# Performance work log

Hardware: AMD Instinct MI355X
Metric: run time of the kernel (lower is better)

The kernel has to match this reference:

```python
import jax, jax.numpy as jnp
import numpy as np

N_HEADS = 16
N_KV_HEADS = 4
HEAD_DIM = 128


def apply_rope(x, cos, sin):
    # x: [b, h, s, head_dim]; cos/sin: [1, 1, s, head_dim//2]
    d = x.shape[-1] // 2
    x1, x2 = x[..., :d], x[..., d:]
    return jnp.concatenate([x1 * cos - x2 * sin, x1 * sin + x2 * cos], axis=-1)


def setup_inputs() -> dict:
    key = jax.random.key(0)
    ks = jax.random.split(key, 9)
    b, s, dim = 2, 2048, 2048
    inp = {
        "x": jax.random.normal(ks[0], (b, s, dim), jnp.float32),
        "cos": jax.random.normal(ks[1], (1, 1, s, HEAD_DIM // 2), jnp.float32),
        "sin": jax.random.normal(ks[2], (1, 1, s, HEAD_DIM // 2), jnp.float32),
        "Wq": jax.random.normal(ks[3], (dim, N_HEADS * HEAD_DIM), jnp.float32) * 0.02,
        "bq": jax.random.normal(ks[4], (N_HEADS * HEAD_DIM,), jnp.float32) * 0.02,
        "Wkv": jax.random.normal(ks[5], (dim, 2 * N_KV_HEADS * HEAD_DIM), jnp.float32) * 0.02,
        "bkv": jax.random.normal(ks[6], (2 * N_KV_HEADS * HEAD_DIM,), jnp.float32) * 0.02,
        "Wo": jax.random.normal(ks[7], (N_HEADS * HEAD_DIM, dim), jnp.float32) * 0.02,
        "bo": jax.random.normal(ks[8], (dim,), jnp.float32) * 0.02,
        "causal": 1,
    }
    return inp


def reference(x, cos, sin, Wq, bq, Wkv, bkv, Wo, bo, causal):
    b, s, dim = x.shape
    scale = 1.0 / np.sqrt(HEAD_DIM)
    # QKV projections (torch Linear with weight stored transposed here)
    q = (x @ Wq + bq).reshape(b, s, N_HEADS, HEAD_DIM).transpose(0, 2, 1, 3)
    kv = x @ Wkv + bkv  # [b, s, 2*n_kv*hd]
    k, v = jnp.split(kv, 2, axis=-1)
    k = k.reshape(b, s, N_KV_HEADS, HEAD_DIM).transpose(0, 2, 1, 3)
    v = v.reshape(b, s, N_KV_HEADS, HEAD_DIM).transpose(0, 2, 1, 3)
    q = apply_rope(q, cos, sin)
    k = apply_rope(k, cos, sin)
    # GQA: repeat kv heads
    rep = N_HEADS // N_KV_HEADS
    k = jnp.repeat(k, rep, axis=1)
    v = jnp.repeat(v, rep, axis=1)
    logits = jnp.einsum("bhqd,bhkd->bhqk", q, k) * scale
    if causal:
        mask = jnp.tril(jnp.ones((s, s), dtype=bool))
        logits = jnp.where(mask[None, None], logits, jnp.finfo(logits.dtype).min)
    scores = jax.nn.softmax(logits, axis=-1)
    vo = jnp.einsum("bhqk,bhkd->bhqd", scores, v)
    vo = vo.transpose(0, 2, 1, 3).reshape(b, s, N_HEADS * HEAD_DIM)
    out = vo @ Wo + bo
    return out
```

## Files before the change

kernel.cpp:

```cpp
#include <hip/hip_runtime.h>
#include <hip/hip_bf16.h>

typedef __bf16 bf16x8 __attribute__((ext_vector_type(8)));
typedef float  f32x4  __attribute__((ext_vector_type(4)));
typedef unsigned int u32;

#define GLD_LDS16(gp, lp) __builtin_amdgcn_global_load_lds( \
    (const __attribute__((address_space(1))) u32*)(gp), \
    (__attribute__((address_space(3))) u32*)(lp), 16, 0, 0)

template<int CTRL>
__device__ __forceinline__ float dpp_rot(float x) {
    int y = __builtin_amdgcn_update_dpp(__float_as_int(x), __float_as_int(x),
                                        CTRL, 0xF, 0xF, false);
    return __int_as_float(y);
}
__device__ __forceinline__ float rowmax16(float x) {
    x = fmaxf(x, dpp_rot<0x121>(x));
    x = fmaxf(x, dpp_rot<0x122>(x));
    x = fmaxf(x, dpp_rot<0x124>(x));
    x = fmaxf(x, dpp_rot<0x128>(x));
    return x;
}
__device__ __forceinline__ float rowsum16(float x) {
    x += dpp_rot<0x121>(x);
    x += dpp_rot<0x122>(x);
    x += dpp_rot<0x124>(x);
    x += dpp_rot<0x128>(x);
    return x;
}


__global__ __launch_bounds__(256) void f32_to_bf16_kernel(
    const float* __restrict__ in, __bf16* __restrict__ out, size_t n) {
    size_t i = ((size_t)blockIdx.x * 256 + threadIdx.x) * 8;
    if (i >= n) return;
    float4 a = *(const float4*)(in + i);
    float4 b = *(const float4*)(in + i + 4);
    bf16x8 v;
    v[0] = (__bf16)a.x; v[1] = (__bf16)a.y; v[2] = (__bf16)a.z; v[3] = (__bf16)a.w;
    v[4] = (__bf16)b.x; v[5] = (__bf16)b.y; v[6] = (__bf16)b.z; v[7] = (__bf16)b.w;
    *(bf16x8*)(out + i) = v;
}

__global__ __launch_bounds__(256) void transpose_to_bf16_kernel(
    const float* __restrict__ W, __bf16* __restrict__ Wt, int K, int N) {
    __shared__ float tile[32][33];
    int n0 = blockIdx.x * 32, k0 = blockIdx.y * 32;
    int tx = threadIdx.x, ty = threadIdx.y;
    #pragma unroll
    for (int i = 0; i < 32; i += 8)
        tile[ty + i][tx] = W[(size_t)(k0 + ty + i) * N + n0 + tx];
    __syncthreads();
    #pragma unroll
    for (int i = 0; i < 32; i += 8)
        Wt[(size_t)(n0 + ty + i) * K + k0 + tx] = (__bf16)tile[tx][ty + i];
}

__global__ __launch_bounds__(256) void concat_bias_kernel(
    const float* __restrict__ bq, const float* __restrict__ bkv,
    float* __restrict__ bqkv) {
    int i = blockIdx.x * 256 + threadIdx.x;
    if (i < 2048) bqkv[i] = bq[i];
    else if (i < 3072) bqkv[i] = bkv[i - 2048];
}

__global__ __launch_bounds__(256) void transpose_v_kernel(
    const __bf16* __restrict__ qkv, __bf16* __restrict__ vtg, int S) {
    __shared__ __bf16 tile[32][33];
    int s0 = blockIdx.x * 32, d0 = blockIdx.y * 32, z = blockIdx.z;
    int b = z >> 2, kvh = z & 3;
    int tx = threadIdx.x, ty = threadIdx.y;
    #pragma unroll
    for (int i = 0; i < 32; i += 8)
        tile[ty + i][tx] =
            qkv[((size_t)b * S + s0 + ty + i) * 3072 + 2560 + kvh * 128 + d0 + tx];
    __syncthreads();
    #pragma unroll
    for (int i = 0; i < 32; i += 8)
        vtg[((size_t)z * 128 + d0 + ty + i) * S + s0 + tx] = tile[tx][ty + i];
}

#define BM 128
#define BN 128
#define BK 64

template <typename OutT>
__global__ __launch_bounds__(256) void gemm_bt_bias_kernel(
    const __bf16* __restrict__ A, const __bf16* __restrict__ Bt,
    const float* __restrict__ bias, OutT* __restrict__ C,
    int M, int N, int K) {
    __shared__ __bf16 As[BM * BK];
    __shared__ __bf16 Bs[BN * BK];
    int tid  = threadIdx.x;
    int nwg  = gridDim.x;
    int cpx  = nwg >> 3;
    int swzb = (blockIdx.x & 7) * cpx + (blockIdx.x >> 3);
    int nbm  = M / BM;
    int bm   = swzb % nbm;
    int bn   = swzb / nbm;
    int wave = tid >> 6;
    int lane = tid & 63;
    int wm   = (wave >> 1) * 64;
    int wn   = (wave & 1) * 64;
    int quad = lane >> 4;
    int l16  = lane & 15;
    int gr   = wave * 32 + (lane >> 3);
    int gc   = (lane & 7) * 8;

    f32x4 acc[4][4];
    f32x4 zero = {0.f, 0.f, 0.f, 0.f};
    #pragma unroll
    for (int i = 0; i < 4; ++i)
        #pragma unroll
        for (int j = 0; j < 4; ++j) acc[i][j] = zero;

    const __bf16* Abase = A  + (size_t)(bm * BM) * K;
    const __bf16* Bbase = Bt + (size_t)(bn * BN) * K;

    for (int k0 = 0; k0 < K; k0 += BK) {
        if (k0) __syncthreads();
        #pragma unroll
        for (int i = 0; i < 4; ++i) {
            GLD_LDS16(Abase + (size_t)(gr + i * 8) * K + k0 + gc,
                      &As[(wave * 32 + i * 8) * BK]);
            GLD_LDS16(Bbase + (size_t)(gr + i * 8) * K + k0 + gc,
                      &Bs[(wave * 32 + i * 8) * BK]);
        }
        __syncthreads();

        bf16x8 af[4][2], bf[4][2];
        #pragma unroll
        for (int i = 0; i < 4; ++i)
            #pragma unroll
            for (int kc = 0; kc < 2; ++kc)
                af[i][kc] = *(bf16x8*)&As[(wm + i * 16 + l16) * BK + kc * 32 + quad * 8];
        #pragma unroll
        for (int j = 0; j < 4; ++j)
            #pragma unroll
            for (int kc = 0; kc < 2; ++kc)
                bf[j][kc] = *(bf16x8*)&Bs[(wn + j * 16 + l16) * BK + kc * 32 + quad * 8];
        #pragma unroll
        for (int kc = 0; kc < 2; ++kc)
            #pragma unroll
            for (int i = 0; i < 4; ++i)
                #pragma unroll
                for (int j = 0; j < 4; ++j)
                    acc[i][j] = __builtin_amdgcn_mfma_f32_16x16x32_bf16(
                        af[i][kc], bf[j][kc], acc[i][j], 0, 0, 0);
    }

    #pragma unroll
    for (int i = 0; i < 4; ++i) {
        int row = bm * BM + wm + i * 16 + quad * 4;
        #pragma unroll
        for (int j = 0; j < 4; ++j) {
            int col  = bn * BN + wn + j * 16 + l16;
            float bv = bias[col];
            #pragma unroll
            for (int r = 0; r < 4; ++r)
                C[(size_t)(row + r) * N + col] = (OutT)(acc[i][j][r] + bv);
        }
    }
}

__global__ __launch_bounds__(256) void rope_kernel(
    __bf16* __restrict__ buf, const float* __restrict__ cosp,
    const float* __restrict__ sinp, int heads, int rowstride, int coloff,
    int S, int total) {
    int idx = blockIdx.x * 256 + threadIdx.x;
    if (idx >= total) return;
    int d  = idx & 63;
    int t2 = idx >> 6;
    int h  = t2 % heads;
    int r  = t2 / heads;
    int s  = r & (S - 1);
    size_t base = (size_t)r * rowstride + coloff + h * 128;
    float x1 = (float)buf[base + d];
    float x2 = (float)buf[base + d + 64];
    float c  = cosp[s * 64 + d];
    float sn = sinp[s * 64 + d];
    buf[base + d]      = (__bf16)(x1 * c - x2 * sn);
    buf[base + d + 64] = (__bf16)(x1 * sn + x2 * c);
}


__global__ __launch_bounds__(256) void flash_mfma_kernel(
    const __bf16* __restrict__ qkv,
    const __bf16* __restrict__ vtg,
    __bf16* __restrict__ vo,
    const int* __restrict__ causal_p, int S) {
    __shared__ __bf16 Ks[2][64 * 128];
    __shared__ __bf16 Vs[2][64 * 128];
    __shared__ __bf16 Ps[4 * 16 * 64];

    const int QKV = 3072;
    int tid  = threadIdx.x;
    int wave = tid >> 6;
    int lane = tid & 63;
    int quad = lane >> 4;
    int l16  = lane & 15;
    int id   = blockIdx.x;
    int xcd  = id & 7;
    int b    = xcd >> 2;
    int kvh  = xcd & 3;
    int rest = id >> 3;
    int hh   = rest & 3;
    int pair = rest >> 2;
    int h    = kvh * 4 + hh;
    int causal = causal_p[0];
    const float SCALE = 0.08838834764831845f;

    const __bf16* vB = vtg + ((size_t)(b * 4 + kvh) * 128) * S;
    char* psw = (char*)Ps + wave * 2048;

    #pragma unroll 1
    for (int phase = 0; phase < 2; ++phase) {
        int qt = phase ? (31 - pair) : pair;
        int q0 = qt * 64;
        int nt = causal ? (qt + 1) : (S / 64);

        bf16x8 a_frag[4];
        size_t qrow = ((size_t)b * S + q0 + wave * 16 + l16) * QKV + h * 128 + quad * 8;
        #pragma unroll
        for (int kc = 0; kc < 4; ++kc)
            a_frag[kc] = *(const bf16x8*)(qkv + qrow + kc * 32);

        f32x4 o_acc[8];
        f32x4 zero4 = {0.f, 0.f, 0.f, 0.f};
        #pragma unroll
        for (int dt = 0; dt < 8; ++dt) o_acc[dt] = zero4;
        float m_[4], l_[4];
        #pragma unroll
        for (int r = 0; r < 4; ++r) { m_[r] = -1e30f; l_[r] = 0.f; }
        int qrow_d = q0 + wave * 16 + quad * 4;

        __syncthreads();
        {
            size_t kg = ((size_t)b * S + wave * 16 + l16) * QKV + 2048 + kvh * 128 + quad * 8;
            #pragma unroll
            for (int kc = 0; kc < 4; ++kc)
                GLD_LDS16(qkv + kg + kc * 32, &Ks[0][(wave * 4 + kc) * 512]);
            #pragma unroll
            for (int i = 0; i < 4; ++i) {
                int c  = wave * 4 + i;
                int dt = c >> 1, kc = c & 1;
                GLD_LDS16(vB + (size_t)(dt * 16 + l16) * S + kc * 32 + quad * 8,
                          &Vs[0][c * 512]);
            }
        }

        for (int t = 0; t < nt; ++t) {
            int cur = t & 1;
            __syncthreads();
            if (t + 1 < nt) {
                size_t kg = ((size_t)b * S + (t + 1) * 64 + wave * 16 + l16) * QKV
                            + 2048 + kvh * 128 + quad * 8;
                #pragma unroll
                for (int kc = 0; kc < 4; ++kc)
                    GLD_LDS16(qkv + kg + kc * 32, &Ks[1 - cur][(wave * 4 + kc) * 512]);
                size_t vgoff = (size_t)(t + 1) * 64;
                #pragma unroll
                for (int i = 0; i < 4; ++i) {
                    int c  = wave * 4 + i;
                    int dt = c >> 1, kc = c & 1;
                    GLD_LDS16(vB + (size_t)(dt * 16 + l16) * S + vgoff + kc * 32 + quad * 8,
                              &Vs[1 - cur][c * 512]);
                }
            }
            int j0 = t * 64;

            f32x4 s_t[4];
            #pragma unroll
            for (int jt = 0; jt < 4; ++jt) s_t[jt] = zero4;
            #pragma unroll
            for (int jt = 0; jt < 4; ++jt)
                #pragma unroll
                for (int kc = 0; kc < 4; ++kc) {
                    bf16x8 kf = *(bf16x8*)&Ks[cur][(jt * 4 + kc) * 512 + lane * 8];
                    s_t[jt] = __builtin_amdgcn_mfma_f32_16x16x32_bf16(
                        a_frag[kc], kf, s_t[jt], 0, 0, 0);
                }

            int diag = causal && (t == nt - 1);
            #pragma unroll
            for (int jt = 0; jt < 4; ++jt)
                #pragma unroll
                for (int r = 0; r < 4; ++r) {
                    float sv = s_t[jt][r] * SCALE;
                    if (diag && (j0 + jt * 16 + l16 > qrow_d + r)) sv = -1e30f;
                    s_t[jt][r] = sv;
                }

            float alpha[4];
            #pragma unroll
            for (int r = 0; r < 4; ++r) {
                float v = fmaxf(fmaxf(s_t[0][r], s_t[1][r]),
                                fmaxf(s_t[2][r], s_t[3][r]));
                v = rowmax16(v);
                float m_new = fmaxf(m_[r], v);
                alpha[r] = __expf(m_[r] - m_new);
                m_[r] = m_new;
                float rs = 0.f;
                #pragma unroll
                for (int jt = 0; jt < 4; ++jt) {
                    float p = __expf(s_t[jt][r] - m_new);
                    s_t[jt][r] = p;
                    rs += p;
                }
                l_[r] = l_[r] * alpha[r] + rs;
            }
            #pragma unroll
            for (int jt = 0; jt < 4; ++jt)
                #pragma unroll
                for (int r = 0; r < 4; ++r) {
                    int prow = quad * 4 + r;
                    int inb  = (jt * 16 + l16) * 2;
                    *(__bf16*)(psw + prow * 128 + (inb ^ ((prow & 7) << 4))) =
                        (__bf16)s_t[jt][r];
                }
            #pragma unroll
            for (int dt = 0; dt < 8; ++dt)
                #pragma unroll
                for (int r = 0; r < 4; ++r) o_acc[dt][r] *= alpha[r];

            int rb  = l16 * 128;
            int swz = (l16 & 7) << 4;
            bf16x8 p0 = *(bf16x8*)(psw + rb + ((quad * 16) ^ swz));
            bf16x8 p1 = *(bf16x8*)(psw + rb + ((64 + quad * 16) ^ swz));
            #pragma unroll
            for (int dt = 0; dt < 8; ++dt) {
                bf16x8 vf0 = *(bf16x8*)&Vs[cur][(dt * 2 + 0) * 512 + lane * 8];
                bf16x8 vf1 = *(bf16x8*)&Vs[cur][(dt * 2 + 1) * 512 + lane * 8];
                o_acc[dt] = __builtin_amdgcn_mfma_f32_16x16x32_bf16(
                    p0, vf0, o_acc[dt], 0, 0, 0);
                o_acc[dt] = __builtin_amdgcn_mfma_f32_16x16x32_bf16(
                    p1, vf1, o_acc[dt], 0, 0, 0);
            }
        }

        float invl[4];
        #pragma unroll
        for (int r = 0; r < 4; ++r) invl[r] = 1.f / rowsum16(l_[r]);
        size_t obase = ((size_t)b * S + q0 + wave * 16 + quad * 4) * 2048
                       + h * 128 + l16;
        #pragma unroll
        for (int dt = 0; dt < 8; ++dt)
            #pragma unroll
            for (int r = 0; r < 4; ++r)
                vo[obase + (size_t)r * 2048 + dt * 16] = (__bf16)(o_acc[dt][r] * invl[r]);
    }
}


extern "C" void kernel_launch(void* const* d_in, const int* in_sizes, int n_in,
                              void* d_out, int out_size, void* d_ws, size_t ws_size,
                              hipStream_t stream) {
    const float* x    = (const float*)d_in[0];
    const float* cosp = (const float*)d_in[1];
    const float* sinp = (const float*)d_in[2];
    const float* Wq   = (const float*)d_in[3];
    const float* bq   = (const float*)d_in[4];
    const float* Wkv  = (const float*)d_in[5];
    const float* bkv  = (const float*)d_in[6];
    const float* Wo   = (const float*)d_in[7];
    const float* bo   = (const float*)d_in[8];
    const int* causal = (const int*)d_in[9];
    float* out = (float*)d_out;

    const int B = 2, S = 2048;
    const int M = B * S;

    char* w = (char*)d_ws;
    __bf16* x16    = (__bf16*)w; w += (size_t)M * 2048 * 2;
    __bf16* Wqkvt  = (__bf16*)w; w += (size_t)3072 * 2048 * 2;
    __bf16* Wot    = (__bf16*)w; w += (size_t)2048 * 2048 * 2;
    float*  bqkv   = (float*)w;  w += (size_t)3072 * 4;
    __bf16* qkvbuf = (__bf16*)w; w += (size_t)M * 3072 * 2;
    __bf16* vobuf  = x16;
    __bf16* vtg    = Wqkvt;

    f32_to_bf16_kernel<<<(M * 2048) / (256 * 8), 256, 0, stream>>>(x, x16, (size_t)M * 2048);
    transpose_to_bf16_kernel<<<dim3(2048 / 32, 2048 / 32), dim3(32, 8), 0, stream>>>(Wq, Wqkvt, 2048, 2048);
    transpose_to_bf16_kernel<<<dim3(1024 / 32, 2048 / 32), dim3(32, 8), 0, stream>>>(Wkv, Wqkvt + (size_t)2048 * 2048, 2048, 1024);
    transpose_to_bf16_kernel<<<dim3(2048 / 32, 2048 / 32), dim3(32, 8), 0, stream>>>(Wo, Wot, 2048, 2048);
    concat_bias_kernel<<<12, 256, 0, stream>>>(bq, bkv, bqkv);
    gemm_bt_bias_kernel<__bf16><<<dim3((M / BM) * (3072 / BN)), 256, 0, stream>>>(x16, Wqkvt, bqkv, qkvbuf, M, 3072, 2048);
    {
        int totq = M * 16 * 64;
        rope_kernel<<<(totq + 255) / 256, 256, 0, stream>>>(qkvbuf, cosp, sinp, 16, 3072, 0, S, totq);
        int totk = M * 4 * 64;
        rope_kernel<<<(totk + 255) / 256, 256, 0, stream>>>(qkvbuf, cosp, sinp, 4, 3072, 2048, S, totk);
    }
    transpose_v_kernel<<<dim3(S / 32, 128 / 32, B * 4), dim3(32, 8), 0, stream>>>(qkvbuf, vtg, S);
    flash_mfma_kernel<<<dim3(512), 256, 0, stream>>>(qkvbuf, vtg, vobuf, causal, S);
    gemm_bt_bias_kernel<float><<<dim3((M / BM) * (2048 / BN)), 256, 0, stream>>>(vobuf, Wot, bo, out, M, 2048, 2048);
}
```

Measured before the change: 393.2 us.

## Fuse prep kernels, fold RoPE and V-transpose into QKV GEMM epilogue

Merges the x conversion, three weight transposes and bias concat into one multi-role prep kernel, cutting launches. The QKV GEMM now stages its output tile in LDS and applies RoPE to Q/K in the epilogue, writing V directly in transposed layout. This removes the separate rope and V-transpose passes and their extra global round-trips, and shrinks the QKV row stride to 2560. It also adds s_setprio around the MFMA blocks in the flash kernel, and gives vtg its own workspace region instead of aliasing the weights.

```diff
diff --git a/kernel.cpp b/kernel.cpp
--- a/kernel.cpp
+++ b/kernel.cpp
@@ -30,68 +30,93 @@
     return x;
 }
 
-
-__global__ __launch_bounds__(256) void f32_to_bf16_kernel(
-    const float* __restrict__ in, __bf16* __restrict__ out, size_t n) {
-    size_t i = ((size_t)blockIdx.x * 256 + threadIdx.x) * 8;
-    if (i >= n) return;
-    float4 a = *(const float4*)(in + i);
-    float4 b = *(const float4*)(in + i + 4);
-    bf16x8 v;
-    v[0] = (__bf16)a.x; v[1] = (__bf16)a.y; v[2] = (__bf16)a.z; v[3] = (__bf16)a.w;
-    v[4] = (__bf16)b.x; v[5] = (__bf16)b.y; v[6] = (__bf16)b.z; v[7] = (__bf16)b.w;
-    *(bf16x8*)(out + i) = v;
-}
-
-__global__ __launch_bounds__(256) void transpose_to_bf16_kernel(
-    const float* __restrict__ W, __bf16* __restrict__ Wt, int K, int N) {
-    __shared__ float tile[32][33];
-    int n0 = blockIdx.x * 32, k0 = blockIdx.y * 32;
-    int tx = threadIdx.x, ty = threadIdx.y;
-    #pragma unroll
-    for (int i = 0; i < 32; i += 8)
-        tile[ty + i][tx] = W[(size_t)(k0 + ty + i) * N + n0 + tx];
-    __syncthreads();
-    #pragma unroll
-    for (int i = 0; i < 32; i += 8)
-        Wt[(size_t)(n0 + ty + i) * K + k0 + tx] = (__bf16)tile[tx][ty + i];
-}
-
-__global__ __launch_bounds__(256) void concat_bias_kernel(
+#define NPREP_A 4096
+#define NPREP_B 4096
+#define NPREP_C 2048
+#define NPREP_D 4096
+#define NPREP_E 12
+
+__global__ __launch_bounds__(256) void prep_kernel(
+    const float* __restrict__ x, __bf16* __restrict__ x16,
+    const float* __restrict__ Wq, const float* __restrict__ Wkv,
+    const float* __restrict__ Wo,
+    __bf16* __restrict__ Wqkvt, __bf16* __restrict__ Wot,
     const float* __restrict__ bq, const float* __restrict__ bkv,
     float* __restrict__ bqkv) {
-    int i = blockIdx.x * 256 + threadIdx.x;
-    if (i < 2048) bqkv[i] = bq[i];
-    else if (i < 3072) bqkv[i] = bkv[i - 2048];
-}
-
-__global__ __launch_bounds__(256) void transpose_v_kernel(
-    const __bf16* __restrict__ qkv, __bf16* __restrict__ vtg, int S) {
-    __shared__ __bf16 tile[32][33];
-    int s0 = blockIdx.x * 32, d0 = blockIdx.y * 32, z = blockIdx.z;
-    int b = z >> 2, kvh = z & 3;
-    int tx = threadIdx.x, ty = threadIdx.y;
-    #pragma unroll
-    for (int i = 0; i < 32; i += 8)
-        tile[ty + i][tx] =
-            qkv[((size_t)b * S + s0 + ty + i) * 3072 + 2560 + kvh * 128 + d0 + tx];
-    __syncthreads();
-    #pragma unroll
-    for (int i = 0; i < 32; i += 8)
-        vtg[((size_t)z * 128 + d0 + ty + i) * S + s0 + tx] = tile[tx][ty + i];
+    __shared__ float tile[32][33];
+    int bid = blockIdx.x;
+    int tid = threadIdx.x;
+
+    if (bid < NPREP_A) {
+        size_t i = (size_t)bid * 2048 + tid * 8;
+        float4 a = *(const float4*)(x + i);
+        float4 b = *(const float4*)(x + i + 4);
+        bf16x8 v;
+        v[0] = (__bf16)a.x; v[1] = (__bf16)a.y; v[2] = (__bf16)a.z; v[3] = (__bf16)a.w;
+        v[4] = (__bf16)b.x; v[5] = (__bf16)b.y; v[6] = (__bf16)b.z; v[7] = (__bf16)b.w;
+        *(bf16x8*)(x16 + i) = v;
+        return;
+    }
+    bid -= NPREP_A;
+    int tx = tid & 31, ty = tid >> 5;
+
+    if (bid < NPREP_B) {
+        int n0 = (bid & 63) * 32, k0 = (bid >> 6) * 32;
+        #pragma unroll
+        for (int i = 0; i < 32; i += 8)
+            tile[ty + i][tx] = Wq[(size_t)(k0 + ty + i) * 2048 + n0 + tx];
+        __syncthreads();
+        #pragma unroll
+        for (int i = 0; i < 32; i += 8)
+            Wqkvt[(size_t)(n0 + ty + i) * 2048 + k0 + tx] = (__bf16)tile[tx][ty + i];
+        return;
+    }
+    bid -= NPREP_B;
+    if (bid < NPREP_C) {
+        int n0 = (bid & 31) * 32, k0 = (bid >> 5) * 32;
+        #pragma unroll
+        for (int i = 0; i < 32; i += 8)
+            tile[ty + i][tx] = Wkv[(size_t)(k0 + ty + i) * 1024 + n0 + tx];
+        __syncthreads();
+        #pragma unroll
+        for (int i = 0; i < 32; i += 8)
+            Wqkvt[(size_t)(2048 + n0 + ty + i) * 2048 + k0 + tx] = (__bf16)tile[tx][ty + i];
+        return;
+    }
+    bid -= NPREP_C;
+    if (bid < NPREP_D) {
+        int n0 = (bid & 63) * 32, k0 = (bid >> 6) * 32;
+        #pragma unroll
+        for (int i = 0; i < 32; i += 8)
+            tile[ty + i][tx] = Wo[(size_t)(k0 + ty + i) * 2048 + n0 + tx];
+        __syncthreads();
+        #pragma unroll
+        for (int i = 0; i < 32; i += 8)
+            Wot[(size_t)(n0 + ty + i) * 2048 + k0 + tx] = (__bf16)tile[tx][ty + i];
+        return;
+    }
+    bid -= NPREP_D;
+    {
+        int i = bid * 256 + tid;
+        if (i < 2048) bqkv[i] = bq[i];
+        else if (i < 3072) bqkv[i] = bkv[i - 2048];
+    }
 }
 
 #define BM 128
 #define BN 128
 #define BK 64
 
-template <typename OutT>
+template <typename OutT, int MODE>
 __global__ __launch_bounds__(256) void gemm_bt_bias_kernel(
     const __bf16* __restrict__ A, const __bf16* __restrict__ Bt,
     const float* __restrict__ bias, OutT* __restrict__ C,
-    int M, int N, int K) {
-    __shared__ __bf16 As[BM * BK];
-    __shared__ __bf16 Bs[BN * BK];
+    int M, int N, int K, int CS,
+    const float* __restrict__ cosp, const float* __restrict__ sinp,
+    __bf16* __restrict__ vtg, int S) {
+    __shared__ __align__(16) char smem[MODE ? (128 * 136 * 2) : (2 * BM * BK * 2)];
+    __bf16* As = (__bf16*)smem;
+    __bf16* Bs = As + BM * BK;
     int tid  = threadIdx.x;
     int nwg  = gridDim.x;
     int cpx  = nwg >> 3;
@@ -150,38 +175,74 @@
                         af[i][kc], bf[j][kc], acc[i][j], 0, 0, 0);
     }
 
-    #pragma unroll
-    for (int i = 0; i < 4; ++i) {
-        int row = bm * BM + wm + i * 16 + quad * 4;
-        #pragma unroll
-        for (int j = 0; j < 4; ++j) {
-            int col  = bn * BN + wn + j * 16 + l16;
-            float bv = bias[col];
-            #pragma unroll
-            for (int r = 0; r < 4; ++r)
-                C[(size_t)(row + r) * N + col] = (OutT)(acc[i][j][r] + bv);
-        }
-    }
-}
-
-__global__ __launch_bounds__(256) void rope_kernel(
-    __bf16* __restrict__ buf, const float* __restrict__ cosp,
-    const float* __restrict__ sinp, int heads, int rowstride, int coloff,
-    int S, int total) {
-    int idx = blockIdx.x * 256 + threadIdx.x;
-    if (idx >= total) return;
-    int d  = idx & 63;
-    int t2 = idx >> 6;
-    int h  = t2 % heads;
-    int r  = t2 / heads;
-    int s  = r & (S - 1);
-    size_t base = (size_t)r * rowstride + coloff + h * 128;
-    float x1 = (float)buf[base + d];
-    float x2 = (float)buf[base + d + 64];
-    float c  = cosp[s * 64 + d];
-    float sn = sinp[s * 64 + d];
-    buf[base + d]      = (__bf16)(x1 * c - x2 * sn);
-    buf[base + d + 64] = (__bf16)(x1 * sn + x2 * c);
+    if constexpr (MODE == 0) {
+        #pragma unroll
+        for (int i = 0; i < 4; ++i) {
+            int row = bm * BM + wm + i * 16 + quad * 4;
+            #pragma unroll
+            for (int j = 0; j < 4; ++j) {
+                int col  = bn * BN + wn + j * 16 + l16;
+                float bv = bias[col];
+                #pragma unroll
+                for (int r = 0; r < 4; ++r)
+                    C[(size_t)(row + r) * N + col] = (OutT)(acc[i][j][r] + bv);
+            }
+        }
+    } else {
+        __syncthreads();
+        __bf16 (*tile)[136] = (__bf16 (*)[136])smem;
+        #pragma unroll
+        for (int i = 0; i < 4; ++i) {
+            int rr = wm + i * 16 + quad * 4;
+            #pragma unroll
+            for (int j = 0; j < 4; ++j) {
+                int cc = wn + j * 16 + l16;
+                float bv = bias[bn * BN + cc];
+                #pragma unroll
+                for (int r = 0; r < 4; ++r)
+                    tile[rr + r][cc] = (__bf16)(acc[i][j][r] + bv);
+            }
+        }
+        __syncthreads();
+
+        if (bn < 20) {
+            #pragma unroll
+            for (int p = 0; p < 4; ++p) {
+                int sr = p * 32 + (tid >> 3);
+                int d0 = (tid & 7) * 8;
+                int grow = bm * BM + sr;
+                int s = grow & (S - 1);
+                const float* cp = cosp + (size_t)s * 64 + d0;
+                const float* sp = sinp + (size_t)s * 64 + d0;
+                bf16x8 r1, r2;
+                #pragma unroll
+                for (int e = 0; e < 8; ++e) {
+                    float x1 = (float)tile[sr][d0 + e];
+                    float x2 = (float)tile[sr][64 + d0 + e];
+                    float c = cp[e], sn = sp[e];
+                    r1[e] = (__bf16)(x1 * c - x2 * sn);
+                    r2[e] = (__bf16)(x1 * sn + x2 * c);
+                }
+                __bf16* outp = (__bf16*)C + (size_t)grow * CS + bn * BN + d0;
+                *(bf16x8*)(outp)      = r1;
+                *(bf16x8*)(outp + 64) = r2;
+            }
+        } else {
+            int kvh = bn - 20;
+            int d  = tid & 127, sg = tid >> 7;
+            #pragma unroll
+            for (int p = 0; p < 8; ++p) {
+                int sl = (p * 2 + sg) * 8;
+                bf16x8 v;
+                #pragma unroll
+                for (int si = 0; si < 8; ++si) v[si] = tile[sl + si][d];
+                int grow = bm * BM + sl;
+                int b = grow >> 11;
+                int s = grow & (S - 1);
+                *(bf16x8*)&vtg[((size_t)(b * 4 + kvh) * 128 + d) * S + s] = v;
+            }
+        }
+    }
 }
 
 
@@ -194,7 +255,7 @@
     __shared__ __bf16 Vs[2][64 * 128];
     __shared__ __bf16 Ps[4 * 16 * 64];
 
-    const int QKV = 3072;
+    const int QKV = 2560;
     int tid  = threadIdx.x;
     int wave = tid >> 6;
     int lane = tid & 63;
@@ -273,6 +334,7 @@
             f32x4 s_t[4];
             #pragma unroll
             for (int jt = 0; jt < 4; ++jt) s_t[jt] = zero4;
+            __builtin_amdgcn_s_setprio(1);
             #pragma unroll
             for (int jt = 0; jt < 4; ++jt)
                 #pragma unroll
@@ -281,6 +343,7 @@
                     s_t[jt] = __builtin_amdgcn_mfma_f32_16x16x32_bf16(
                         a_frag[kc], kf, s_t[jt], 0, 0, 0);
                 }
+            __builtin_amdgcn_s_setprio(0);
 
             int diag = causal && (t == nt - 1);
             #pragma unroll
@@ -328,6 +391,7 @@
             int swz = (l16 & 7) << 4;
             bf16x8 p0 = *(bf16x8*)(psw + rb + ((quad * 16) ^ swz));
             bf16x8 p1 = *(bf16x8*)(psw + rb + ((64 + quad * 16) ^ swz));
+            __builtin_amdgcn_s_setprio(1);
             #pragma unroll
             for (int dt = 0; dt < 8; ++dt) {
                 bf16x8 vf0 = *(bf16x8*)&Vs[cur][(dt * 2 + 0) * 512 + lane * 8];
@@ -337,6 +401,7 @@
                 o_acc[dt] = __builtin_amdgcn_mfma_f32_16x16x32_bf16(
                     p1, vf1, o_acc[dt], 0, 0, 0);
             }
+            __builtin_amdgcn_s_setprio(0);
         }
 
         float invl[4];
@@ -376,23 +441,15 @@
     __bf16* Wqkvt  = (__bf16*)w; w += (size_t)3072 * 2048 * 2;
     __bf16* Wot    = (__bf16*)w; w += (size_t)2048 * 2048 * 2;
     float*  bqkv   = (float*)w;  w += (size_t)3072 * 4;
-    __bf16* qkvbuf = (__bf16*)w; w += (size_t)M * 3072 * 2;
+    __bf16* qkvbuf = (__bf16*)w; w += (size_t)M * 2560 * 2;
+    __bf16* vtg    = (__bf16*)w; w += (size_t)8 * 128 * S * 2;
     __bf16* vobuf  = x16;
-    __bf16* vtg    = Wqkvt;
-
-    f32_to_bf16_kernel<<<(M * 2048) / (256 * 8), 256, 0, stream>>>(x, x16, (size_t)M * 2048);
-    transpose_to_bf16_kernel<<<dim3(2048 / 32, 2048 / 32), dim3(32, 8), 0, stream>>>(Wq, Wqkvt, 2048, 2048);
-    transpose_to_bf16_kernel<<<dim3(1024 / 32, 2048 / 32), dim3(32, 8), 0, stream>>>(Wkv, Wqkvt + (size_t)2048 * 2048, 2048, 1024);
-    transpose_to_bf16_kernel<<<dim3(2048 / 32, 2048 / 32), dim3(32, 8), 0, stream>>>(Wo, Wot, 2048, 2048);
-    concat_bias_kernel<<<12, 256, 0, stream>>>(bq, bkv, bqkv);
-    gemm_bt_bias_kernel<__bf16><<<dim3((M / BM) * (3072 / BN)), 256, 0, stream>>>(x16, Wqkvt, bqkv, qkvbuf, M, 3072, 2048);
-    {
-        int totq = M * 16 * 64;
-        rope_kernel<<<(totq + 255) / 256, 256, 0, stream>>>(qkvbuf, cosp, sinp, 16, 3072, 0, S, totq);
-        int totk = M * 4 * 64;
-        rope_kernel<<<(totk + 255) / 256, 256, 0, stream>>>(qkvbuf, cosp, sinp, 4, 3072, 2048, S, totk);
-    }
-    transpose_v_kernel<<<dim3(S / 32, 128 / 32, B * 4), dim3(32, 8), 0, stream>>>(qkvbuf, vtg, S);
+
+    prep_kernel<<<dim3(NPREP_A + NPREP_B + NPREP_C + NPREP_D + NPREP_E), 256, 0, stream>>>(
+        x, x16, Wq, Wkv, Wo, Wqkvt, Wot, bq, bkv, bqkv);
+    gemm_bt_bias_kernel<__bf16, 1><<<dim3((M / BM) * (3072 / BN)), 256, 0, stream>>>(
+        x16, Wqkvt, bqkv, qkvbuf, M, 3072, 2048, 2560, cosp, sinp, vtg, S);
     flash_mfma_kernel<<<dim3(512), 256, 0, stream>>>(qkvbuf, vtg, vobuf, causal, S);
-    gemm_bt_bias_kernel<float><<<dim3((M / BM) * (2048 / BN)), 256, 0, stream>>>(vobuf, Wot, bo, out, M, 2048, 2048);
-}
+    gemm_bt_bias_kernel<float, 0><<<dim3((M / BM) * (2048 / BN)), 256, 0, stream>>>(
+        vobuf, Wot, bo, out, M, 2048, 2048, 2048, nullptr, nullptr, nullptr, S);
+}
```

After: 371.4 us. -5.5%, faster.
